# Kernel optimization log

Measured on AMD Instinct MI355X. Metric: run time of the kernel, lower is better.

## Reference

```python
import jax, jax.numpy as jnp
import numpy as np

DT = 0.02
N_STEPS = 50
BATCH = 131072
DIM = 3


def setup_inputs() -> dict:
    key = jax.random.key(0)
    ks = jax.random.split(key, 10)

    def lin(k, fan_in, fan_out):
        return jax.random.normal(k, (fan_in, fan_out), jnp.float32) / jnp.sqrt(jnp.float32(fan_in))

    return {
        "y0": jax.random.normal(ks[0], (DIM,), jnp.float32),
        "Y0": jnp.zeros((1, 1), jnp.float32),
        "qW1": lin(ks[1], DIM + 1, 64), "qb1": jnp.zeros((64,), jnp.float32),
        "qW2": lin(ks[2], 64, 64),      "qb2": jnp.zeros((64,), jnp.float32),
        "qW3": lin(ks[3], 64, 1),       "qb3": jnp.zeros((1,), jnp.float32),
        "zW1": lin(ks[4], DIM + 1, 64), "zb1": jnp.zeros((64,), jnp.float32),
        "zW2": lin(ks[5], 64, 64),      "zb2": jnp.zeros((64,), jnp.float32),
        "zW3": lin(ks[6], 64, 3),       "zb3": jnp.zeros((3,), jnp.float32),
        # pre-drawn standard normals; scaled by sqrt(dt) inside reference
        "dW": jax.random.normal(ks[7], (N_STEPS, BATCH, 3), jnp.float32),
    }


def _mlp(x, W1, b1, W2, b2, W3, b3):
    h = jax.nn.relu(x @ W1 + b1)
    h = jax.nn.relu(h @ W2 + b2)
    return h @ W3 + b3


def reference(y0, Y0, qW1, qb1, qW2, qb2, qW3, qb3,
              zW1, zb1, zW2, zb2, zW3, zb3, dW):
    n_steps, B, _ = dW.shape
    dt = jnp.float32(DT)
    sqrt_dt = jnp.sqrt(dt)
    eye3 = jnp.eye(DIM, dtype=y0.dtype)

    y_init = jnp.broadcast_to(y0[None, :], (B, DIM))
    Y_init = jnp.broadcast_to(Y0, (B, 1))
    ts = jnp.arange(n_steps, dtype=y0.dtype) * dt

    def step(carry, xs):
        y, Y, res = carry
        t_scalar, dWn = xs
        t = jnp.full((B, 1), t_scalar, dtype=y.dtype)
        x = jnp.concatenate([t, y], axis=1)                      # [B, dim+1]
        z = _mlp(x, zW1, zb1, zW2, zb2, zW3, zb3)                # [B, 3]
        q = _mlp(x, qW1, qb1, qW2, qb2, qW3, qb3)                # [B, 1]
        f = 0.5 * q ** 2                                         # generator
        dWs = dWn * sqrt_dt                                      # [B, 3]
        mu = -y + q                                              # drift, [B, dim]
        sigma = (0.2 + 0.1 * jnp.tanh(y))[:, :, None] * eye3     # [B, dim, 3]
        diffusion = jnp.einsum('bij,bj->bi', sigma, dWs)
        y_next = y + mu * dt + diffusion
        Y_next = Y - f * dt + jnp.sum(z * dWs, axis=1, keepdims=True)
        # residual = detach(Y_next) - (Y - f*dt + (z*dW).sum()) == 0 identically
        residual = jax.lax.stop_gradient(Y_next - Y_next)
        res = res + jnp.mean(residual ** 2)
        return (y_next, Y_next, res), None

    (y, Y, total_res), _ = jax.lax.scan(
        step, (y_init, Y_init, jnp.float32(0.0)), (ts, dW))
    terminal = jnp.sum(y ** 2, axis=1, keepdims=True)            # terminal cost
    return jnp.mean((Y - terminal) ** 2) + total_res
```

## Files before the change

kernel.cpp:

```cpp
#include <hip/hip_runtime.h>
#include <math.h>

#define N_STEPS 50
#define DT 0.02f

typedef __attribute__((ext_vector_type(8))) short    bf16x8;
typedef __attribute__((ext_vector_type(4))) float    f32x4;
typedef __attribute__((ext_vector_type(4))) unsigned u32x4;

__device__ inline unsigned f2bf(float f) {
    unsigned u = __builtin_bit_cast(unsigned, f);
    return ((u + 0x7FFFu + ((u >> 16) & 1u)) >> 16);
}
__device__ inline unsigned pk2(float lo, float hi) {
    return (f2bf(lo) & 0xFFFFu) | (f2bf(hi) << 16);
}
__device__ inline unsigned cvtpk(float lo, float hi) {
    unsigned r;
    asm("v_cvt_pk_bf16_f32 %0, %1, %2" : "=v"(r) : "v"(lo), "v"(hi));
    return r;
}
__device__ inline bf16x8 mk8(unsigned a, unsigned b, unsigned cc, unsigned d) {
    u32x4 t; t.x = a; t.y = b; t.z = cc; t.w = d;
    return __builtin_bit_cast(bf16x8, t);
}

__global__ __launch_bounds__(128, 2) void bsde_kernel(
    const float* __restrict__ y0v, const float* __restrict__ Y0v,
    const float* __restrict__ qW1, const float* __restrict__ qb1,
    const float* __restrict__ qW2, const float* __restrict__ qb2,
    const float* __restrict__ qW3, const float* __restrict__ qb3,
    const float* __restrict__ zW1, const float* __restrict__ zb1,
    const float* __restrict__ zW2, const float* __restrict__ zb2,
    const float* __restrict__ zW3, const float* __restrict__ zb3,
    const float* __restrict__ dW,
    float* __restrict__ out, int B)
{
    const int lane = threadIdx.x & 63;
    const int net  = threadIdx.x >> 6;
    const int c    = lane & 15;
    const int g    = lane >> 4;
    const int p    = blockIdx.x * 64 + lane;

    __shared__ unsigned short ex[2][4096];
    __shared__ float qbuf[2][64];
    __shared__ f32x4 w3t[2][64];

    const float* W1 = net ? qW1 : zW1;
    const float* b1 = net ? qb1 : zb1;
    const float* W2 = net ? qW2 : zW2;
    const float* b2 = net ? qb2 : zb2;
    const float* W3 = net ? qW3 : zW3;
    const float* b3 = net ? qb3 : zb3;

    if (net) w3t[1][lane] = (f32x4){W3[lane], 0.f, 0.f, 0.f};
    else     w3t[0][lane] = (f32x4){W3[3*lane+0], W3[3*lane+1], W3[3*lane+2], 0.f};

    bf16x8 w1f[4];
#pragma unroll
    for (int mt = 0; mt < 4; ++mt) {
        const int h = 16 * mt + c;
        unsigned d0 = 0, d1 = 0, d2 = 0;
        if (g == 0) {
            d0 = pk2(W1[0 * 64 + h], W1[1 * 64 + h]);
            d1 = pk2(W1[2 * 64 + h], W1[3 * 64 + h]);
            d2 = f2bf(b1[h]) & 0xFFFFu;
        }
        w1f[mt] = mk8(d0, d1, d2, 0);
    }

    bf16x8 w2f[4][2];
#pragma unroll
    for (int mt = 0; mt < 4; ++mt)
#pragma unroll
    for (int kt = 0; kt < 2; ++kt) {
        const int h = 16 * mt + c;
        const int k0 = 32 * kt + 8 * g;
        unsigned d0 = pk2(W2[(k0 + 0) * 64 + h], W2[(k0 + 1) * 64 + h]);
        unsigned d1 = pk2(W2[(k0 + 2) * 64 + h], W2[(k0 + 3) * 64 + h]);
        unsigned d2 = pk2(W2[(k0 + 4) * 64 + h], W2[(k0 + 5) * 64 + h]);
        unsigned d3 = pk2(W2[(k0 + 6) * 64 + h], W2[(k0 + 7) * 64 + h]);
        w2f[mt][kt] = mk8(d0, d1, d2, d3);
    }

    f32x4 b2v[4];
#pragma unroll
    for (int mt = 0; mt < 4; ++mt)
#pragma unroll
    for (int r = 0; r < 4; ++r)
        b2v[mt][r] = b2[16 * mt + 4 * g + r];

    __syncthreads();

    char* exn = (char*)&ex[net][0];
    const int sw = (c & 7) << 4;
    const unsigned jp2c = (g == 0) ? 0x3F80u : 0u;

    const float sqrt_dt = sqrtf(DT);
    float y0 = y0v[0], y1 = y0v[1], y2 = y0v[2];
    float Y  = Y0v[0];

    for (int n = 0; n < N_STEPS; ++n) {
        const float t  = (float)n * DT;
        const int   bu = n & 1;

        const size_t idx = ((size_t)n * (size_t)B + (size_t)p) * 3;
        const float dr0 = dW[idx + 0];
        const float dr1 = dW[idx + 1];
        const float dr2 = dW[idx + 2];

#pragma unroll
        for (int t4 = 0; t4 < 4; ++t4) {
            const int src = 16 * t4 + c;
            const float s0 = __shfl(y0, src, 64);
            const float s1 = __shfl(y1, src, 64);
            const float s2 = __shfl(y2, src, 64);
            const unsigned a = cvtpk(t,  s0);
            const unsigned b = cvtpk(s1, s2);
            const bf16x8 xf = mk8((g == 0) ? a : 0u, (g == 0) ? b : 0u, jp2c, 0u);
#pragma unroll
            for (int mt = 0; mt < 4; ++mt) {
                f32x4 c1 = __builtin_amdgcn_mfma_f32_16x16x32_bf16(
                    w1f[mt], xf, (f32x4){0.f, 0.f, 0.f, 0.f}, 0, 0, 0);
                const unsigned lo = cvtpk(fmaxf(c1[0], 0.f), fmaxf(c1[1], 0.f));
                const unsigned hi = cvtpk(fmaxf(c1[2], 0.f), fmaxf(c1[3], 0.f));
                const int off = (((16 * t4 + c) * 128) + 32 * mt + 8 * g) ^ sw;
                *(unsigned long long*)(exn + off) =
                    ((unsigned long long)hi << 32) | (unsigned long long)lo;
            }
        }

        float p0[4] = {0.f, 0.f, 0.f, 0.f};
        float p1[4] = {0.f, 0.f, 0.f, 0.f};
        float p2[4] = {0.f, 0.f, 0.f, 0.f};
#pragma unroll
        for (int t4 = 0; t4 < 4; ++t4) {
            const int rb = ((16 * t4 + c) * 128) + 16 * g;
            const bf16x8 hf0 = *(const bf16x8*)(exn + ((rb +  0) ^ sw));
            const bf16x8 hf1 = *(const bf16x8*)(exn + ((rb + 64) ^ sw));
#pragma unroll
            for (int mt = 0; mt < 4; ++mt) {
                f32x4 acc = __builtin_amdgcn_mfma_f32_16x16x32_bf16(
                    w2f[mt][0], hf0, b2v[mt], 0, 0, 0);
                acc = __builtin_amdgcn_mfma_f32_16x16x32_bf16(
                    w2f[mt][1], hf1, acc, 0, 0, 0);
#pragma unroll
                for (int r = 0; r < 4; ++r) {
                    const float h = fmaxf(acc[r], 0.f);
                    const f32x4 w3r = w3t[net][16 * mt + 4 * g + r];
                    p0[t4] = fmaf(h, w3r[0], p0[t4]);
                    if (net == 0) {
                        p1[t4] = fmaf(h, w3r[1], p1[t4]);
                        p2[t4] = fmaf(h, w3r[2], p2[t4]);
                    }
                }
            }
        }

        float out0, oz1 = 0.f, oz2 = 0.f;
        {
            float r4[4];
#pragma unroll
            for (int t4 = 0; t4 < 4; ++t4) {
                float v = p0[t4];
                v += __shfl_xor(v, 16, 64);
                v += __shfl_xor(v, 32, 64);
                r4[t4] = v;
            }
            float pick = r4[0];
            pick = (g == 1) ? r4[1] : pick;
            pick = (g == 2) ? r4[2] : pick;
            pick = (g == 3) ? r4[3] : pick;
            out0 = pick + b3[0];
        }
        if (net == 0) {
            float r4[4];
#pragma unroll
            for (int t4 = 0; t4 < 4; ++t4) {
                float v = p1[t4];
                v += __shfl_xor(v, 16, 64);
                v += __shfl_xor(v, 32, 64);
                r4[t4] = v;
            }
            float pick = r4[0];
            pick = (g == 1) ? r4[1] : pick;
            pick = (g == 2) ? r4[2] : pick;
            pick = (g == 3) ? r4[3] : pick;
            oz1 = pick + b3[1];
#pragma unroll
            for (int t4 = 0; t4 < 4; ++t4) {
                float v = p2[t4];
                v += __shfl_xor(v, 16, 64);
                v += __shfl_xor(v, 32, 64);
                r4[t4] = v;
            }
            pick = r4[0];
            pick = (g == 1) ? r4[1] : pick;
            pick = (g == 2) ? r4[2] : pick;
            pick = (g == 3) ? r4[3] : pick;
            oz2 = pick + b3[2];
        }

        if (net == 1) qbuf[bu][lane] = out0;
        __syncthreads();
        const float qq = net ? out0 : qbuf[bu][lane];

        const float dw0 = dr0 * sqrt_dt;
        const float dw1 = dr1 * sqrt_dt;
        const float dw2 = dr2 * sqrt_dt;

        if (net == 0) {
            const float f = 0.5f * qq * qq;
            Y = Y - f * DT + (out0 * dw0 + oz1 * dw1 + oz2 * dw2);
        }

        const float s0 = 0.2f + 0.1f * tanhf(y0);
        const float s1 = 0.2f + 0.1f * tanhf(y1);
        const float s2 = 0.2f + 0.1f * tanhf(y2);
        y0 = y0 + (qq - y0) * DT + s0 * dw0;
        y1 = y1 + (qq - y1) * DT + s1 * dw1;
        y2 = y2 + (qq - y2) * DT + s2 * dw2;
    }

    if (net == 0) {
        const float term = y0 * y0 + y1 * y1 + y2 * y2;
        const float d    = Y - term;
        float val = d * d;
#pragma unroll
        for (int off = 32; off > 0; off >>= 1)
            val += __shfl_down(val, off, 64);
        if (lane == 0)
            atomicAdd(out, val * (1.0f / (float)B));
    }
}

extern "C" void kernel_launch(void* const* d_in, const int* in_sizes, int n_in,
                              void* d_out, int out_size, void* d_ws, size_t ws_size,
                              hipStream_t stream) {
    const float* y0  = (const float*)d_in[0];
    const float* Y0  = (const float*)d_in[1];
    const float* qW1 = (const float*)d_in[2];
    const float* qb1 = (const float*)d_in[3];
    const float* qW2 = (const float*)d_in[4];
    const float* qb2 = (const float*)d_in[5];
    const float* qW3 = (const float*)d_in[6];
    const float* qb3 = (const float*)d_in[7];
    const float* zW1 = (const float*)d_in[8];
    const float* zb1 = (const float*)d_in[9];
    const float* zW2 = (const float*)d_in[10];
    const float* zb2 = (const float*)d_in[11];
    const float* zW3 = (const float*)d_in[12];
    const float* zb3 = (const float*)d_in[13];
    const float* dW  = (const float*)d_in[14];

    const int B = in_sizes[14] / (N_STEPS * 3);
    float* out = (float*)d_out;

    hipMemsetAsync(out, 0, sizeof(float), stream);

    const int threads = 128;
    const int blocks  = B / 64;
    bsde_kernel<<<blocks, threads, 0, stream>>>(
        y0, Y0, qW1, qb1, qW2, qb2, qW3, qb3,
        zW1, zb1, zW2, zb2, zW3, zb3, dW, out, B);
}
```

Measured before the change: 445.5 us.

## Merge z and q networks into one wavefront per block, drop per-step barrier

Each block now runs one 64-lane wavefront that evaluates both MLPs, holding 8 weight tiles in registers, rather than two wavefronts that each ran one network and swapped q through shared memory with a __syncthreads every step. This removes the per-step barrier and the duplicated y-update and tanh work across the two waves. The layer-3 weights are stored column-major so they load as vectors, and tanhf is replaced by an exp/rcp approximation. The cost is roughly double register pressure per wave, which may lower occupancy, plus twice the serial MFMA work per wave and a slightly less accurate tanh.

```diff
diff --git a/kernel.cpp b/kernel.cpp
--- a/kernel.cpp
+++ b/kernel.cpp
@@ -24,8 +24,30 @@
     u32x4 t; t.x = a; t.y = b; t.z = cc; t.w = d;
     return __builtin_bit_cast(bf16x8, t);
 }
-
-__global__ __launch_bounds__(128, 2) void bsde_kernel(
+__device__ inline float fast_tanh(float x) {
+    float e, r;
+    asm("v_exp_f32 %0, %1" : "=v"(e) : "v"(x * 2.8853900817779268f));
+    asm("v_rcp_f32 %0, %1" : "=v"(r) : "v"(e + 1.0f));
+    return fmaf(-2.0f, r, 1.0f);
+}
+
+__device__ inline float red4(const float pv[4], int g) {
+    float r4[4];
+#pragma unroll
+    for (int t4 = 0; t4 < 4; ++t4) {
+        float v = pv[t4];
+        v += __shfl_xor(v, 16, 64);
+        v += __shfl_xor(v, 32, 64);
+        r4[t4] = v;
+    }
+    float pick = r4[0];
+    pick = (g == 1) ? r4[1] : pick;
+    pick = (g == 2) ? r4[2] : pick;
+    pick = (g == 3) ? r4[3] : pick;
+    return pick;
+}
+
+__global__ __launch_bounds__(64, 2) void bsde_kernel(
     const float* __restrict__ y0v, const float* __restrict__ Y0v,
     const float* __restrict__ qW1, const float* __restrict__ qb1,
     const float* __restrict__ qW2, const float* __restrict__ qb2,
@@ -36,30 +58,25 @@
     const float* __restrict__ dW,
     float* __restrict__ out, int B)
 {
-    const int lane = threadIdx.x & 63;
-    const int net  = threadIdx.x >> 6;
+    const int lane = threadIdx.x;
     const int c    = lane & 15;
     const int g    = lane >> 4;
     const int p    = blockIdx.x * 64 + lane;
 
-    __shared__ unsigned short ex[2][4096];
-    __shared__ float qbuf[2][64];
-    __shared__ f32x4 w3t[2][64];
-
-    const float* W1 = net ? qW1 : zW1;
-    const float* b1 = net ? qb1 : zb1;
-    const float* W2 = net ? qW2 : zW2;
-    const float* b2 = net ? qb2 : zb2;
-    const float* W3 = net ? qW3 : zW3;
-    const float* b3 = net ? qb3 : zb3;
-
-    if (net) w3t[1][lane] = (f32x4){W3[lane], 0.f, 0.f, 0.f};
-    else     w3t[0][lane] = (f32x4){W3[3*lane+0], W3[3*lane+1], W3[3*lane+2], 0.f};
-
-    bf16x8 w1f[4];
-#pragma unroll
-    for (int mt = 0; mt < 4; ++mt) {
-        const int h = 16 * mt + c;
+    __shared__ unsigned short ex[64 * 128];
+    __shared__ __align__(16) float w3c[4][64];
+
+    w3c[0][lane] = zW3[3 * lane + 0];
+    w3c[1][lane] = zW3[3 * lane + 1];
+    w3c[2][lane] = zW3[3 * lane + 2];
+    w3c[3][lane] = qW3[lane];
+
+    bf16x8 w1f[8];
+#pragma unroll
+    for (int mt = 0; mt < 8; ++mt) {
+        const float* W1 = (mt < 4) ? zW1 : qW1;
+        const float* b1 = (mt < 4) ? zb1 : qb1;
+        const int h = 16 * (mt & 3) + c;
         unsigned d0 = 0, d1 = 0, d2 = 0;
         if (g == 0) {
             d0 = pk2(W1[0 * 64 + h], W1[1 * 64 + h]);
@@ -69,30 +86,37 @@
         w1f[mt] = mk8(d0, d1, d2, 0);
     }
 
-    bf16x8 w2f[4][2];
-#pragma unroll
-    for (int mt = 0; mt < 4; ++mt)
-#pragma unroll
-    for (int kt = 0; kt < 2; ++kt) {
-        const int h = 16 * mt + c;
-        const int k0 = 32 * kt + 8 * g;
-        unsigned d0 = pk2(W2[(k0 + 0) * 64 + h], W2[(k0 + 1) * 64 + h]);
-        unsigned d1 = pk2(W2[(k0 + 2) * 64 + h], W2[(k0 + 3) * 64 + h]);
-        unsigned d2 = pk2(W2[(k0 + 4) * 64 + h], W2[(k0 + 5) * 64 + h]);
-        unsigned d3 = pk2(W2[(k0 + 6) * 64 + h], W2[(k0 + 7) * 64 + h]);
-        w2f[mt][kt] = mk8(d0, d1, d2, d3);
-    }
-
-    f32x4 b2v[4];
-#pragma unroll
-    for (int mt = 0; mt < 4; ++mt)
-#pragma unroll
-    for (int r = 0; r < 4; ++r)
-        b2v[mt][r] = b2[16 * mt + 4 * g + r];
+    bf16x8 w2f[8][2];
+#pragma unroll
+    for (int mt = 0; mt < 8; ++mt) {
+        const float* W2 = (mt < 4) ? zW2 : qW2;
+        const int h = 16 * (mt & 3) + c;
+#pragma unroll
+        for (int kt = 0; kt < 2; ++kt) {
+            const int k0 = 32 * kt + 8 * g;
+            w2f[mt][kt] = mk8(
+                pk2(W2[(k0 + 0) * 64 + h], W2[(k0 + 1) * 64 + h]),
+                pk2(W2[(k0 + 2) * 64 + h], W2[(k0 + 3) * 64 + h]),
+                pk2(W2[(k0 + 4) * 64 + h], W2[(k0 + 5) * 64 + h]),
+                pk2(W2[(k0 + 6) * 64 + h], W2[(k0 + 7) * 64 + h]));
+        }
+    }
+
+    f32x4 b2v[8];
+#pragma unroll
+    for (int mt = 0; mt < 8; ++mt) {
+        const float* b2 = (mt < 4) ? zb2 : qb2;
+#pragma unroll
+        for (int r = 0; r < 4; ++r)
+            b2v[mt][r] = b2[16 * (mt & 3) + 4 * g + r];
+    }
+
+    const float zb3_0 = zb3[0], zb3_1 = zb3[1], zb3_2 = zb3[2];
+    const float qb3_0 = qb3[0];
 
     __syncthreads();
 
-    char* exn = (char*)&ex[net][0];
+    char* exn = (char*)ex;
     const int sw = (c & 7) << 4;
     const unsigned jp2c = (g == 0) ? 0x3F80u : 0u;
 
@@ -101,8 +125,7 @@
     float Y  = Y0v[0];
 
     for (int n = 0; n < N_STEPS; ++n) {
-        const float t  = (float)n * DT;
-        const int   bu = n & 1;
+        const float t = (float)n * DT;
 
         const size_t idx = ((size_t)n * (size_t)B + (size_t)p) * 3;
         const float dr0 = dW[idx + 0];
@@ -119,27 +142,38 @@
             const unsigned b = cvtpk(s1, s2);
             const bf16x8 xf = mk8((g == 0) ? a : 0u, (g == 0) ? b : 0u, jp2c, 0u);
 #pragma unroll
-            for (int mt = 0; mt < 4; ++mt) {
+            for (int mt = 0; mt < 8; ++mt) {
                 f32x4 c1 = __builtin_amdgcn_mfma_f32_16x16x32_bf16(
                     w1f[mt], xf, (f32x4){0.f, 0.f, 0.f, 0.f}, 0, 0, 0);
                 const unsigned lo = cvtpk(fmaxf(c1[0], 0.f), fmaxf(c1[1], 0.f));
                 const unsigned hi = cvtpk(fmaxf(c1[2], 0.f), fmaxf(c1[3], 0.f));
-                const int off = (((16 * t4 + c) * 128) + 32 * mt + 8 * g) ^ sw;
+                const int off = (((16 * t4 + c) * 256) + (mt >> 2) * 128
+                                 + 32 * (mt & 3) + 8 * g) ^ sw;
                 *(unsigned long long*)(exn + off) =
                     ((unsigned long long)hi << 32) | (unsigned long long)lo;
             }
         }
 
-        float p0[4] = {0.f, 0.f, 0.f, 0.f};
-        float p1[4] = {0.f, 0.f, 0.f, 0.f};
-        float p2[4] = {0.f, 0.f, 0.f, 0.f};
-#pragma unroll
-        for (int t4 = 0; t4 < 4; ++t4) {
-            const int rb = ((16 * t4 + c) * 128) + 16 * g;
-            const bf16x8 hf0 = *(const bf16x8*)(exn + ((rb +  0) ^ sw));
-            const bf16x8 hf1 = *(const bf16x8*)(exn + ((rb + 64) ^ sw));
-#pragma unroll
-            for (int mt = 0; mt < 4; ++mt) {
+        float pz0[4] = {0.f, 0.f, 0.f, 0.f};
+        float pz1[4] = {0.f, 0.f, 0.f, 0.f};
+        float pz2[4] = {0.f, 0.f, 0.f, 0.f};
+        float pq [4] = {0.f, 0.f, 0.f, 0.f};
+#pragma unroll
+        for (int mt = 0; mt < 8; ++mt) {
+            const int hb = 16 * (mt & 3) + 4 * g;
+            f32x4 wz0, wz1, wz2, wq;
+            if (mt < 4) {
+                wz0 = *(const f32x4*)&w3c[0][hb];
+                wz1 = *(const f32x4*)&w3c[1][hb];
+                wz2 = *(const f32x4*)&w3c[2][hb];
+            } else {
+                wq  = *(const f32x4*)&w3c[3][hb];
+            }
+#pragma unroll
+            for (int t4 = 0; t4 < 4; ++t4) {
+                const int rb = ((16 * t4 + c) * 256) + (mt >> 2) * 128 + 16 * g;
+                const bf16x8 hf0 = *(const bf16x8*)(exn + ((rb +  0) ^ sw));
+                const bf16x8 hf1 = *(const bf16x8*)(exn + ((rb + 64) ^ sw));
                 f32x4 acc = __builtin_amdgcn_mfma_f32_16x16x32_bf16(
                     w2f[mt][0], hf0, b2v[mt], 0, 0, 0);
                 acc = __builtin_amdgcn_mfma_f32_16x16x32_bf16(
@@ -147,91 +181,45 @@
 #pragma unroll
                 for (int r = 0; r < 4; ++r) {
                     const float h = fmaxf(acc[r], 0.f);
-                    const f32x4 w3r = w3t[net][16 * mt + 4 * g + r];
-                    p0[t4] = fmaf(h, w3r[0], p0[t4]);
-                    if (net == 0) {
-                        p1[t4] = fmaf(h, w3r[1], p1[t4]);
-                        p2[t4] = fmaf(h, w3r[2], p2[t4]);
+                    if (mt < 4) {
+                        pz0[t4] = fmaf(h, wz0[r], pz0[t4]);
+                        pz1[t4] = fmaf(h, wz1[r], pz1[t4]);
+                        pz2[t4] = fmaf(h, wz2[r], pz2[t4]);
+                    } else {
+                        pq[t4]  = fmaf(h, wq[r],  pq[t4]);
                     }
                 }
             }
         }
 
-        float out0, oz1 = 0.f, oz2 = 0.f;
-        {
-            float r4[4];
-#pragma unroll
-            for (int t4 = 0; t4 < 4; ++t4) {
-                float v = p0[t4];
-                v += __shfl_xor(v, 16, 64);
-                v += __shfl_xor(v, 32, 64);
-                r4[t4] = v;
-            }
-            float pick = r4[0];
-            pick = (g == 1) ? r4[1] : pick;
-            pick = (g == 2) ? r4[2] : pick;
-            pick = (g == 3) ? r4[3] : pick;
-            out0 = pick + b3[0];
-        }
-        if (net == 0) {
-            float r4[4];
-#pragma unroll
-            for (int t4 = 0; t4 < 4; ++t4) {
-                float v = p1[t4];
-                v += __shfl_xor(v, 16, 64);
-                v += __shfl_xor(v, 32, 64);
-                r4[t4] = v;
-            }
-            float pick = r4[0];
-            pick = (g == 1) ? r4[1] : pick;
-            pick = (g == 2) ? r4[2] : pick;
-            pick = (g == 3) ? r4[3] : pick;
-            oz1 = pick + b3[1];
-#pragma unroll
-            for (int t4 = 0; t4 < 4; ++t4) {
-                float v = p2[t4];
-                v += __shfl_xor(v, 16, 64);
-                v += __shfl_xor(v, 32, 64);
-                r4[t4] = v;
-            }
-            pick = r4[0];
-            pick = (g == 1) ? r4[1] : pick;
-            pick = (g == 2) ? r4[2] : pick;
-            pick = (g == 3) ? r4[3] : pick;
-            oz2 = pick + b3[2];
-        }
-
-        if (net == 1) qbuf[bu][lane] = out0;
-        __syncthreads();
-        const float qq = net ? out0 : qbuf[bu][lane];
+        const float oz0 = red4(pz0, g) + zb3_0;
+        const float oz1 = red4(pz1, g) + zb3_1;
+        const float oz2 = red4(pz2, g) + zb3_2;
+        const float qq  = red4(pq,  g) + qb3_0;
 
         const float dw0 = dr0 * sqrt_dt;
         const float dw1 = dr1 * sqrt_dt;
         const float dw2 = dr2 * sqrt_dt;
 
-        if (net == 0) {
-            const float f = 0.5f * qq * qq;
-            Y = Y - f * DT + (out0 * dw0 + oz1 * dw1 + oz2 * dw2);
-        }
-
-        const float s0 = 0.2f + 0.1f * tanhf(y0);
-        const float s1 = 0.2f + 0.1f * tanhf(y1);
-        const float s2 = 0.2f + 0.1f * tanhf(y2);
+        const float f = 0.5f * qq * qq;
+        Y = Y - f * DT + (oz0 * dw0 + oz1 * dw1 + oz2 * dw2);
+
+        const float s0 = 0.2f + 0.1f * fast_tanh(y0);
+        const float s1 = 0.2f + 0.1f * fast_tanh(y1);
+        const float s2 = 0.2f + 0.1f * fast_tanh(y2);
         y0 = y0 + (qq - y0) * DT + s0 * dw0;
         y1 = y1 + (qq - y1) * DT + s1 * dw1;
         y2 = y2 + (qq - y2) * DT + s2 * dw2;
     }
 
-    if (net == 0) {
-        const float term = y0 * y0 + y1 * y1 + y2 * y2;
-        const float d    = Y - term;
-        float val = d * d;
-#pragma unroll
-        for (int off = 32; off > 0; off >>= 1)
-            val += __shfl_down(val, off, 64);
-        if (lane == 0)
-            atomicAdd(out, val * (1.0f / (float)B));
-    }
+    const float term = y0 * y0 + y1 * y1 + y2 * y2;
+    const float d    = Y - term;
+    float val = d * d;
+#pragma unroll
+    for (int off = 32; off > 0; off >>= 1)
+        val += __shfl_down(val, off, 64);
+    if (lane == 0)
+        atomicAdd(out, val * (1.0f / (float)B));
 }
 
 extern "C" void kernel_launch(void* const* d_in, const int* in_sizes, int n_in,
@@ -258,7 +246,7 @@
 
     hipMemsetAsync(out, 0, sizeof(float), stream);
 
-    const int threads = 128;
+    const int threads = 64;
     const int blocks  = B / 64;
     bsde_kernel<<<blocks, threads, 0, stream>>>(
         y0, Y0, qW1, qb1, qW2, qb2, qW3, qb3,
```

New measurement: 400.6 us. 10.1% less time.
